# Performance work log

Measured on AMD Instinct MI355X. Metric: run time of the kernel, lower is better.

The kernel has to match this reference:

```python
import jax, jax.numpy as jnp
import numpy as np

NPOINT = 1024
RADIUS = 0.2
NSAMPLE = 32
EPS = 1e-5  # BatchNorm eps


def setup_inputs() -> dict:
    key = jax.random.key(0)
    ks = jax.random.split(key, 8)
    B, N, D = 16, 4096, 64
    xyz = jax.random.uniform(ks[0], (B, N, 3), dtype=jnp.float32)
    points = jax.random.normal(ks[1], (B, N, D), dtype=jnp.float32)
    chans = [D + 3, 64, 64, 128]  # last_channel = in_channel + 3
    inp = {"xyz": xyz, "points": points}
    for i in range(3):
        inp[f"W{i}"] = jax.random.normal(ks[2 + i], (chans[i + 1], chans[i]), dtype=jnp.float32) * 0.05
        inp[f"b{i}"] = jnp.zeros((chans[i + 1],), jnp.float32)
        inp[f"g{i}"] = jnp.ones((chans[i + 1],), jnp.float32)
        inp[f"bt{i}"] = jnp.zeros((chans[i + 1],), jnp.float32)
    return inp


def farthest_point_sample(xyz, npoint):
    # xyz: [B, N, 3] -> idx [B, npoint]. Deterministic start at index 0.
    B, N, _ = xyz.shape

    def body(carry, _):
        distance, farthest = carry
        centroid = jnp.take_along_axis(xyz, farthest[:, None, None], axis=1)  # [B,1,3]
        dist = jnp.sum((xyz - centroid) ** 2, axis=-1)  # [B,N]
        distance = jnp.minimum(distance, dist)
        nxt = jnp.argmax(distance, axis=1).astype(jnp.int32)
        return (distance, nxt), farthest

    init = (jnp.full((B, N), 1e10, xyz.dtype), jnp.zeros((B,), jnp.int32))
    _, idx = jax.lax.scan(body, init, None, length=npoint)
    return idx.T  # [B, npoint]


def query_ball_point(radius, nsample, xyz, new_xyz):
    # squared distances [B,S,N] via |a|^2 + |b|^2 - 2ab (no [B,S,N,3] blowup)
    sqr = (jnp.sum(new_xyz ** 2, -1)[:, :, None]
           + jnp.sum(xyz ** 2, -1)[:, None, :]
           - 2.0 * jnp.einsum('bsc,bnc->bsn', new_xyz, xyz))
    neg_d, idx = jax.lax.top_k(-sqr, nsample)  # k smallest dists, sorted ascending
    mask = (-neg_d) > radius ** 2
    return jnp.where(mask, idx[:, :, :1], idx)  # replace out-of-ball with nearest


def _gather(points, idx):
    # points [B,N,C], idx [B,...] -> [B,...,C]
    return jax.vmap(lambda p, i: p[i])(points, idx)


def reference(xyz, points, W0, b0, g0, bt0, W1, b1, g1, bt1, W2, b2, g2, bt2):
    fps_idx = farthest_point_sample(xyz, NPOINT)                 # [B,S]
    new_xyz = jnp.take_along_axis(xyz, fps_idx[:, :, None], axis=1)  # [B,S,3]
    idx = query_ball_point(RADIUS, NSAMPLE, xyz, new_xyz)        # [B,S,K]
    grouped_xyz = _gather(xyz, idx)                              # [B,S,K,3]
    grouped_xyz_norm = grouped_xyz - new_xyz[:, :, None, :]
    x = jnp.concatenate([grouped_xyz_norm, _gather(points, idx)], axis=-1)  # [B,S,K,C]

    # 1x1 conv + BatchNorm (training-mode batch stats over B,S,K) + ReLU
    for W, b, ga, be in ((W0, b0, g0, bt0), (W1, b1, g1, bt1), (W2, b2, g2, bt2)):
        x = jnp.einsum('bskc,oc->bsko', x, W) + b
        mu = jnp.mean(x, axis=(0, 1, 2))
        var = jnp.var(x, axis=(0, 1, 2))
        x = ga * (x - mu) * jax.lax.rsqrt(var + EPS) + be
        x = jax.nn.relu(x)

    new_points = jnp.max(x, axis=2)  # max-pool over K -> [B,S,C_out]
    return (new_xyz, new_points)
```

## Files before the change

kernel.cpp:

```cpp
#include <hip/hip_runtime.h>

typedef unsigned int u32;
typedef unsigned long long u64;
typedef unsigned short ushort_t;

#define NB 16
#define NPT 4096
#define NS 1024
#define NK 32
#define ND 64
#define CNT_TOTAL 524288.0f
#define OUT_NP_OFF 49152

__device__ __forceinline__ u64 wave_min_u64_bcast(u64 x) {
  #define DPP_MINU64(CTRL) {                                                  \
    int hi = (int)(x >> 32), lo = (int)(u32)x;                                \
    int h2 = __builtin_amdgcn_update_dpp(hi, hi, CTRL, 0xf, 0xf, false);      \
    int l2 = __builtin_amdgcn_update_dpp(lo, lo, CTRL, 0xf, 0xf, false);      \
    u64 y = ((u64)(u32)h2 << 32) | (u32)l2;                                   \
    if (y < x) x = y; }
  DPP_MINU64(0x111) DPP_MINU64(0x112) DPP_MINU64(0x114) DPP_MINU64(0x118)
  DPP_MINU64(0x142) DPP_MINU64(0x143)
  #undef DPP_MINU64
  u32 hi = (u32)__builtin_amdgcn_readlane((int)(x >> 32), 63);
  u32 lo = (u32)__builtin_amdgcn_readlane((int)(u32)x, 63);
  return ((u64)hi << 32) | lo;
}

__device__ __forceinline__ double wave_max_f64(double x) {
  #define DPP_MAXF64(CTRL) {                                                  \
    int hi = __double2hiint(x), lo = __double2loint(x);                       \
    int h2 = __builtin_amdgcn_update_dpp(hi, hi, CTRL, 0xf, 0xf, false);      \
    int l2 = __builtin_amdgcn_update_dpp(lo, lo, CTRL, 0xf, 0xf, false);      \
    x = fmax(x, __hiloint2double(h2, l2)); }
  DPP_MAXF64(0x111) DPP_MAXF64(0x112) DPP_MAXF64(0x114) DPP_MAXF64(0x118)
  DPP_MAXF64(0x142) DPP_MAXF64(0x143)
  #undef DPP_MAXF64
  return x;
}

__global__ __launch_bounds__(256) void k_fps(const float* __restrict__ xyz,
                                             float* __restrict__ out_xyz) {
  __shared__ float sx[NPT], sy[NPT], sz[NPT];
  __shared__ u64 wkey[2][4];
  const int b = blockIdx.x, t = threadIdx.x;
  const int lane = t & 63, w = t >> 6;
  const float* xb = xyz + (size_t)b * NPT * 3;
  float px[16], py[16], pz[16], dst[16];
  {
    float f[48];
    const float4* s4 = (const float4*)(xb + t * 48);
    #pragma unroll
    for (int j = 0; j < 12; ++j) {
      float4 v = s4[j];
      f[4*j+0] = v.x; f[4*j+1] = v.y; f[4*j+2] = v.z; f[4*j+3] = v.w;
    }
    #pragma unroll
    for (int k = 0; k < 16; ++k) {
      px[k] = f[3*k+0]; py[k] = f[3*k+1]; pz[k] = f[3*k+2]; dst[k] = 1e10f;
      const int n = t * 16 + k;
      sx[n] = px[k]; sy[n] = py[k]; sz[n] = pz[k];
    }
  }
  __syncthreads();
  float fx = xb[0], fy = xb[1], fz = xb[2];
  float* ob = out_xyz + (size_t)b * NS * 3;
  const int lobase = NPT - 1 - t * 16;
  for (int it = 0; it < NS; ++it) {
    if (t == 0) { ob[3*it+0] = fx; ob[3*it+1] = fy; ob[3*it+2] = fz; }
    double kk[16];
    #pragma unroll
    for (int k = 0; k < 16; ++k) {
      float dx = __fsub_rn(px[k], fx), dy = __fsub_rn(py[k], fy), dz = __fsub_rn(pz[k], fz);
      float dd = __fadd_rn(__fadd_rn(__fmul_rn(dx,dx), __fmul_rn(dy,dy)), __fmul_rn(dz,dz));
      dd = fminf(dst[k], dd);
      dst[k] = dd;
      kk[k] = __hiloint2double(__float_as_int(dd), lobase - k);
    }
    #pragma unroll
    for (int s = 8; s >= 1; s >>= 1)
      #pragma unroll
      for (int i = 0; i < 16; ++i) { if (i < s) kk[i] = fmax(kk[i], kk[i + s]); }
    double wm = wave_max_f64(kk[0]);
    const int p = it & 1;
    if (lane == 63) wkey[p][w] = ((u64)(u32)__double2hiint(wm) << 32) | (u32)__double2loint(wm);
    __syncthreads();
    u64 m0 = wkey[p][0], m1 = wkey[p][1], m2 = wkey[p][2], m3 = wkey[p][3];
    u64 ma = m0 > m1 ? m0 : m1, mb = m2 > m3 ? m2 : m3;
    u64 m = ma > mb ? ma : mb;
    const int idx = NPT - 1 - (int)(m & 0xffffffffu);
    fx = sx[idx]; fy = sy[idx]; fz = sz[idx];
  }
}

#define SQCAP 1024
__global__ __launch_bounds__(256) void k_ball(const float* __restrict__ xyz,
                                              const float* __restrict__ nxyz,
                                              ushort_t* __restrict__ ballidx) {
  __shared__ u64 keys[4][SQCAP];
  const int w = threadIdx.x >> 6, lane = threadIdx.x & 63;
  const int pair = blockIdx.x * 4 + w;
  const int b = pair >> 10;
  const float* xb = xyz + (size_t)b * NPT * 3;
  const float nx = nxyz[(size_t)pair*3+0];
  const float ny = nxyz[(size_t)pair*3+1];
  const float nz = nxyz[(size_t)pair*3+2];
  const float ssn = __fadd_rn(__fadd_rn(__fmul_rn(nx,nx), __fmul_rn(ny,ny)), __fmul_rn(nz,nz));
  int cnt = 0;
  for (int n0 = 0; n0 < NPT; n0 += 64) {
    const int n = n0 + lane;
    const float px = xb[3*n+0], py = xb[3*n+1], pz = xb[3*n+2];
    const float ssx = __fadd_rn(__fadd_rn(__fmul_rn(px,px), __fmul_rn(py,py)), __fmul_rn(pz,pz));
    const float dt  = __fadd_rn(__fadd_rn(__fmul_rn(nx,px), __fmul_rn(ny,py)), __fmul_rn(nz,pz));
    const float d   = __fsub_rn(__fadd_rn(ssn, ssx), __fmul_rn(2.0f, dt));
    const bool in = !(d > 0.04f);
    const u64 mask = __ballot(in);
    if (in) {
      int pos = cnt + (int)__popcll(mask & ((1ull << lane) - 1ull));
      if (pos < SQCAP) {
        u32 bits = __float_as_uint(d);
        u32 mapped = (bits & 0x80000000u) ? ~bits : (bits | 0x80000000u);
        keys[w][pos] = ((u64)mapped << 32) | (u32)n;
      }
    }
    cnt += (int)__popcll(mask);
  }
  if (cnt > SQCAP) cnt = SQCAP;
  ushort_t* op = ballidx + (size_t)pair * NK;
  int first = 0;
  volatile u64* kp = &keys[w][0];
  for (int iter = 0; iter < NK; ++iter) {
    if (iter < cnt) {
      u64 mb = ~0ull;
      for (int i = lane; i < cnt; i += 64) { u64 kk = kp[i]; if (kk < mb) mb = kk; }
      mb = wave_min_u64_bcast(mb);
      for (int i = lane; i < cnt; i += 64) { if (kp[i] == mb) kp[i] = ~0ull; }
      const int widx = (int)(mb & 0xffffffffu);
      if (iter == 0) first = widx;
      if (lane == 0) op[iter] = (ushort_t)widx;
    } else {
      if (lane == 0) op[iter] = (ushort_t)first;
    }
  }
}

template<int ROWS, int K, int LDW>
__device__ __forceinline__ void load_W(float* Ws, const float* __restrict__ W, int t) {
  for (int e = t; e < ROWS * K; e += 256) Ws[(e / K) * LDW + (e % K)] = W[e];
}

__device__ __forceinline__ void gather_X(float (*Xs)[69],
    const float* __restrict__ xyz, const float* __restrict__ points,
    const float* __restrict__ nxyz, const ushort_t* __restrict__ ballidx,
    int bp4, int b, int t) {
  if (t < 128) {
    const int pair = bp4 + (t >> 5);
    const int idx = (int)ballidx[pair * NK + (t & 31)];
    const float* p = xyz + ((size_t)b * NPT + idx) * 3;
    const float* nzp = nxyz + (size_t)pair * 3;
    Xs[t][0] = __fsub_rn(p[0], nzp[0]);
    Xs[t][1] = __fsub_rn(p[1], nzp[1]);
    Xs[t][2] = __fsub_rn(p[2], nzp[2]);
  }
  for (int g = t; g < 2048; g += 256) {
    const int r = g >> 4, ch = g & 15;
    const int pair = bp4 + (r >> 5);
    const int idx = (int)ballidx[pair * NK + (r & 31)];
    float4 v = *(const float4*)(points + ((size_t)b * NPT + idx) * ND + ch * 4);
    Xs[r][3 + ch*4 + 0] = v.x; Xs[r][3 + ch*4 + 1] = v.y;
    Xs[r][3 + ch*4 + 2] = v.z; Xs[r][3 + ch*4 + 3] = v.w;
  }
}

template<int K, int LDW>
__device__ __forceinline__ void gemm4(const float (*Xs)[69], const float* Ws,
                                      const float* __restrict__ bias, int biasOff,
                                      int tr, int tc, float acc[8][4]) {
  #pragma unroll
  for (int j = 0; j < 4; ++j) {
    float bb = bias[biasOff + tc*4 + j];
    #pragma unroll
    for (int i = 0; i < 8; ++i) acc[i][j] = bb;
  }
  for (int c = 0; c < K; ++c) {
    float wv[4];
    #pragma unroll
    for (int j = 0; j < 4; ++j) wv[j] = Ws[(tc*4 + j) * LDW + c];
    #pragma unroll
    for (int i = 0; i < 8; ++i) {
      float xv = Xs[tr*8 + i][c];
      #pragma unroll
      for (int j = 0; j < 4; ++j) acc[i][j] = fmaf(xv, wv[j], acc[i][j]);
    }
  }
}

__device__ __forceinline__ void bn_coef(const float* __restrict__ stats, int base,
    const float* __restrict__ g, const float* __restrict__ bt,
    float* sc, float* sh, int t) {
  if (t < 64) {
    const float inv = 1.0f / CNT_TOTAL;
    float mu = stats[base + t] * inv;
    float var = fmaxf(stats[base + 64 + t] * inv - mu * mu, 0.0f);
    float rs = rsqrtf(var + 1e-5f);
    float s = g[t] * rs;
    sc[t] = s; sh[t] = bt[t] - mu * s;
  }
}

__device__ __forceinline__ void load_y_bn(float (*Xs)[69], const float* __restrict__ y,
    size_t row0, const float* sc, const float* sh, int t) {
  for (int g = t; g < 2048; g += 256) {
    const int r = g >> 4, ch = g & 15;
    float4 v = *(const float4*)(y + (row0 + r) * 64 + ch * 4);
    const int c = ch * 4;
    Xs[r][c+0] = fmaxf(fmaf(sc[c+0], v.x, sh[c+0]), 0.0f);
    Xs[r][c+1] = fmaxf(fmaf(sc[c+1], v.y, sh[c+1]), 0.0f);
    Xs[r][c+2] = fmaxf(fmaf(sc[c+2], v.z, sh[c+2]), 0.0f);
    Xs[r][c+3] = fmaxf(fmaf(sc[c+3], v.w, sh[c+3]), 0.0f);
  }
}

__device__ __forceinline__ void bn_to_Xs(float (*Xs)[69], float acc[8][4],
    const float* sc, const float* sh, int tr, int tc) {
  #pragma unroll
  for (int j = 0; j < 4; ++j) {
    int c = tc*4 + j;
    #pragma unroll
    for (int i = 0; i < 8; ++i)
      Xs[tr*8 + i][c] = fmaxf(fmaf(sc[c], acc[i][j], sh[c]), 0.0f);
  }
}

__device__ __forceinline__ void store_y(float* __restrict__ y, size_t row0,
                                        float acc[8][4], int tr, int tc) {
  #pragma unroll
  for (int i = 0; i < 8; ++i) {
    size_t gr = row0 + tr*8 + i;
    *(float4*)(y + gr * 64 + tc*4) = make_float4(acc[i][0], acc[i][1], acc[i][2], acc[i][3]);
  }
}

__device__ __forceinline__ void stats_acc64(float acc[8][4], float* ssum, float* ssq,
    float* __restrict__ gsum, float* __restrict__ gsq, int tc, int t) {
  #pragma unroll
  for (int j = 0; j < 4; ++j) {
    float s0 = 0.f, s1 = 0.f;
    #pragma unroll
    for (int i = 0; i < 8; ++i) { s0 += acc[i][j]; s1 += acc[i][j]*acc[i][j]; }
    atomicAdd(&ssum[tc*4 + j], s0);
    atomicAdd(&ssq [tc*4 + j], s1);
  }
  __syncthreads();
  if (t < 64) { atomicAdd(&gsum[t], ssum[t]); atomicAdd(&gsq[t], ssq[t]); }
}

template<bool STORE>
__global__ __launch_bounds__(256) void k_pass0(const float* __restrict__ xyz,
    const float* __restrict__ points, const float* __restrict__ nxyz,
    const ushort_t* __restrict__ ballidx, const float* __restrict__ W0,
    const float* __restrict__ b0, float* __restrict__ y0, float* __restrict__ stats) {
  __shared__ float Xs[128][69];
  __shared__ float Ws[64*69];
  __shared__ float ssum[64], ssq[64];
  const int t = threadIdx.x;
  const int bp4 = blockIdx.x * 4, b = bp4 >> 10;
  const size_t row0 = (size_t)blockIdx.x * 128;
  if (t < 64) { ssum[t] = 0.f; ssq[t] = 0.f; }
  load_W<64,67,69>(Ws, W0, t);
  gather_X(Xs, xyz, points, nxyz, ballidx, bp4, b, t);
  __syncthreads();
  const int tr = t >> 4, tc = t & 15;
  float acc[8][4];
  gemm4<67,69>(Xs, Ws, b0, 0, tr, tc, acc);
  if (STORE) store_y(y0, row0, acc, tr, tc);
  stats_acc64(acc, ssum, ssq, stats, stats + 64, tc, t);
}

template<bool LOADY0, bool STORE>
__global__ __launch_bounds__(256) void k_pass1(const float* __restrict__ xyz,
    const float* __restrict__ points, const float* __restrict__ nxyz,
    const ushort_t* __restrict__ ballidx,
    const float* __restrict__ W0, const float* __restrict__ b0,
    const float* __restrict__ g0, const float* __restrict__ bt0,
    const float* __restrict__ W1, const float* __restrict__ b1,
    const float* __restrict__ y0, float* __restrict__ y1, float* __restrict__ stats) {
  __shared__ float Xs[128][69];
  __shared__ float Ws[64*69];
  __shared__ float sc[64], sh[64], ssum[64], ssq[64];
  const int t = threadIdx.x;
  const int bp4 = blockIdx.x * 4, b = bp4 >> 10;
  const size_t row0 = (size_t)blockIdx.x * 128;
  if (t < 64) { ssum[t] = 0.f; ssq[t] = 0.f; }
  bn_coef(stats, 0, g0, bt0, sc, sh, t);
  const int tr = t >> 4, tc = t & 15;
  if (LOADY0) {
    load_W<64,64,69>(Ws, W1, t);
    __syncthreads();
    load_y_bn(Xs, y0, row0, sc, sh, t);
    __syncthreads();
  } else {
    load_W<64,67,69>(Ws, W0, t);
    gather_X(Xs, xyz, points, nxyz, ballidx, bp4, b, t);
    __syncthreads();
    float a0[8][4];
    gemm4<67,69>(Xs, Ws, b0, 0, tr, tc, a0);
    __syncthreads();
    bn_to_Xs(Xs, a0, sc, sh, tr, tc);
    load_W<64,64,69>(Ws, W1, t);
    __syncthreads();
  }
  float acc[8][4];
  gemm4<64,69>(Xs, Ws, b1, 0, tr, tc, acc);
  if (STORE) store_y(y1, row0, acc, tr, tc);
  stats_acc64(acc, ssum, ssq, stats + 128, stats + 192, tc, t);
}

template<int MODE>
__global__ __launch_bounds__(256) void k_pass2(const float* __restrict__ xyz,
    const float* __restrict__ points, const float* __restrict__ nxyz,
    const ushort_t* __restrict__ ballidx,
    const float* __restrict__ W0, const float* __restrict__ b0,
    const float* __restrict__ g0, const float* __restrict__ bt0,
    const float* __restrict__ W1, const float* __restrict__ b1,
    const float* __restrict__ g1, const float* __restrict__ bt1,
    const float* __restrict__ W2, const float* __restrict__ b2,
    const float* __restrict__ g2,
    const float* __restrict__ y0, const float* __restrict__ y1,
    float* __restrict__ out, float* __restrict__ stats) {
  __shared__ float Xs[128][69];
  __shared__ float Ws[64*69];
  __shared__ float plex[16*64];
  __shared__ float sc0[64], sh0[64], sc1[64], sh1[64];
  __shared__ float ssum[128], ssq[128], sg[128];
  const int t = threadIdx.x;
  const int bp4 = blockIdx.x * 4, b = bp4 >> 10;
  const size_t row0 = (size_t)blockIdx.x * 128;
  if (t < 128) { ssum[t] = 0.f; ssq[t] = 0.f; sg[t] = g2[t]; }
  bn_coef(stats, 128, g1, bt1, sc1, sh1, t);
  const int tr = t >> 4, tc = t & 15;
  if (MODE == 0) {
    load_y_bn(Xs, y1, row0, sc1, sh1, t);
  } else {
    bn_coef(stats, 0, g0, bt0, sc0, sh0, t);
    if (MODE == 1) {
      load_W<64,64,69>(Ws, W1, t);
      __syncthreads();
      load_y_bn(Xs, y0, row0, sc0, sh0, t);
      __syncthreads();
    } else {
      load_W<64,67,69>(Ws, W0, t);
      gather_X(Xs, xyz, points, nxyz, ballidx, bp4, b, t);
      __syncthreads();
      float a0[8][4];
      gemm4<67,69>(Xs, Ws, b0, 0, tr, tc, a0);
      __syncthreads();
      bn_to_Xs(Xs, a0, sc0, sh0, tr, tc);
      load_W<64,64,69>(Ws, W1, t);
      __syncthreads();
    }
    float a1[8][4];
    gemm4<64,69>(Xs, Ws, b1, 0, tr, tc, a1);
    __syncthreads();
    bn_to_Xs(Xs, a1, sc1, sh1, tr, tc);
  }
  for (int h = 0; h < 2; ++h) {
    load_W<64,64,65>(Ws, W2 + h * 64 * 64, t);
    __syncthreads();
    float acc[8][4];
    gemm4<64,65>(Xs, Ws, b2, h * 64, tr, tc, acc);
    #pragma unroll
    for (int j = 0; j < 4; ++j) {
      float s0 = 0.f, s1 = 0.f;
      #pragma unroll
      for (int i = 0; i < 8; ++i) { s0 += acc[i][j]; s1 += acc[i][j]*acc[i][j]; }
      atomicAdd(&ssum[h*64 + tc*4 + j], s0);
      atomicAdd(&ssq [h*64 + tc*4 + j], s1);
    }
    #pragma unroll
    for (int j = 0; j < 4; ++j) {
      const bool useMax = sg[h*64 + tc*4 + j] >= 0.0f;
      float e = acc[0][j];
      #pragma unroll
      for (int i = 1; i < 8; ++i) e = useMax ? fmaxf(e, acc[i][j]) : fminf(e, acc[i][j]);
      plex[tr * 64 + tc*4 + j] = e;
    }
    __syncthreads();
    {
      const int pl = t >> 6, o = t & 63;
      const bool useMax = sg[h*64 + o] >= 0.0f;
      float e = plex[(pl*4 + 0) * 64 + o];
      #pragma unroll
      for (int i = 1; i < 4; ++i) {
        float v = plex[(pl*4 + i) * 64 + o];
        e = useMax ? fmaxf(e, v) : fminf(e, v);
      }
      out[OUT_NP_OFF + (size_t)(bp4 + pl) * 128 + h*64 + o] = e;
    }
  }
  __syncthreads();
  if (t < 128) { atomicAdd(&stats[256 + t], ssum[t]); atomicAdd(&stats[384 + t], ssq[t]); }
}

__global__ __launch_bounds__(256) void k_final(const float* __restrict__ stats,
                                               const float* __restrict__ g2,
                                               const float* __restrict__ bt2,
                                               float* __restrict__ out) {
  const int gid = blockIdx.x * 256 + threadIdx.x;
  const int o = gid & 127;
  const float inv = 1.0f / CNT_TOTAL;
  float mu = stats[256 + o] * inv;
  float var = fmaxf(stats[384 + o] * inv - mu * mu, 0.0f);
  float rs = rsqrtf(var + 1e-5f);
  float s = g2[o] * rs;
  float b = bt2[o] - mu * s;
  float v = out[OUT_NP_OFF + gid];
  out[OUT_NP_OFF + gid] = fmaxf(fmaf(s, v, b), 0.0f);
}

extern "C" void kernel_launch(void* const* d_in, const int* in_sizes, int n_in,
                              void* d_out, int out_size, void* d_ws, size_t ws_size,
                              hipStream_t stream) {
  (void)in_sizes; (void)n_in; (void)out_size;
  const float* xyz    = (const float*)d_in[0];
  const float* points = (const float*)d_in[1];
  const float* W0  = (const float*)d_in[2];
  const float* b0  = (const float*)d_in[3];
  const float* g0  = (const float*)d_in[4];
  const float* bt0 = (const float*)d_in[5];
  const float* W1  = (const float*)d_in[6];
  const float* b1  = (const float*)d_in[7];
  const float* g1  = (const float*)d_in[8];
  const float* bt1 = (const float*)d_in[9];
  const float* W2  = (const float*)d_in[10];
  const float* b2  = (const float*)d_in[11];
  const float* g2  = (const float*)d_in[12];
  const float* bt2 = (const float*)d_in[13];
  float* out = (float*)d_out;

  const size_t statsB = 2048;
  const size_t ballB  = (size_t)16384 * NK * 2;
  const size_t MINWS  = statsB + ballB;
  const size_t yB     = (size_t)524288 * 64 * 4;

  char* ws = (char*)d_ws;
  float* stats      = (float*)ws;
  ushort_t* ballidx = (ushort_t*)(ws + statsB);
  float* y0         = (float*)(ws + MINWS);
  float* y1         = (float*)(ws + MINWS + yB);

  hipMemsetAsync(stats, 0, statsB, stream);
  k_fps <<<dim3(NB),   dim3(256),  0, stream>>>(xyz, out);
  k_ball<<<dim3(4096), dim3(256),  0, stream>>>(xyz, out, ballidx);

  if (ws_size >= MINWS + 2 * yB) {
    k_pass0<true>        <<<dim3(4096), dim3(256), 0, stream>>>(xyz, points, out, ballidx, W0, b0, y0, stats);
    k_pass1<true, true>  <<<dim3(4096), dim3(256), 0, stream>>>(xyz, points, out, ballidx, W0, b0, g0, bt0, W1, b1, y0, y1, stats);
    k_pass2<0>           <<<dim3(4096), dim3(256), 0, stream>>>(xyz, points, out, ballidx, W0, b0, g0, bt0, W1, b1, g1, bt1, W2, b2, g2, y0, y1, out, stats);
  } else if (ws_size >= MINWS + yB) {
    k_pass0<true>        <<<dim3(4096), dim3(256), 0, stream>>>(xyz, points, out, ballidx, W0, b0, y0, stats);
    k_pass1<true, false> <<<dim3(4096), dim3(256), 0, stream>>>(xyz, points, out, ballidx, W0, b0, g0, bt0, W1, b1, y0, y1, stats);
    k_pass2<1>           <<<dim3(4096), dim3(256), 0, stream>>>(xyz, points, out, ballidx, W0, b0, g0, bt0, W1, b1, g1, bt1, W2, b2, g2, y0, y1, out, stats);
  } else {
    k_pass0<false>       <<<dim3(4096), dim3(256), 0, stream>>>(xyz, points, out, ballidx, W0, b0, y0, stats);
    k_pass1<false, false><<<dim3(4096), dim3(256), 0, stream>>>(xyz, points, out, ballidx, W0, b0, g0, bt0, W1, b1, y0, y1, stats);
    k_pass2<2>           <<<dim3(4096), dim3(256), 0, stream>>>(xyz, points, out, ballidx, W0, b0, g0, bt0, W1, b1, g1, bt1, W2, b2, g2, y0, y1, out, stats);
  }
  k_final<<<dim3(8192), dim3(256), 0, stream>>>(stats, g2, bt2, out);
}
```

Measured before the change: 1.432 ms.

## Widen FPS blocks to 512 threads and keep ball-query candidates in registers

```diff
diff --git a/kernel.cpp b/kernel.cpp
--- a/kernel.cpp
+++ b/kernel.cpp
@@ -39,38 +39,37 @@
   return x;
 }
 
-__global__ __launch_bounds__(256) void k_fps(const float* __restrict__ xyz,
+__global__ __launch_bounds__(512) void k_fps(const float* __restrict__ xyz,
                                              float* __restrict__ out_xyz) {
   __shared__ float sx[NPT], sy[NPT], sz[NPT];
-  __shared__ u64 wkey[2][4];
+  __shared__ u64 wkey[2][8];
   const int b = blockIdx.x, t = threadIdx.x;
   const int lane = t & 63, w = t >> 6;
   const float* xb = xyz + (size_t)b * NPT * 3;
-  float px[16], py[16], pz[16], dst[16];
+  float px[8], py[8], pz[8], dst[8];
   {
-    float f[48];
-    const float4* s4 = (const float4*)(xb + t * 48);
-    #pragma unroll
-    for (int j = 0; j < 12; ++j) {
-      float4 v = s4[j];
-      f[4*j+0] = v.x; f[4*j+1] = v.y; f[4*j+2] = v.z; f[4*j+3] = v.w;
-    }
-    #pragma unroll
-    for (int k = 0; k < 16; ++k) {
-      px[k] = f[3*k+0]; py[k] = f[3*k+1]; pz[k] = f[3*k+2]; dst[k] = 1e10f;
-      const int n = t * 16 + k;
+    const float4* s4 = (const float4*)(xb + t * 24);
+    float4 v0 = s4[0], v1 = s4[1], v2 = s4[2], v3 = s4[3], v4 = s4[4], v5 = s4[5];
+    px[0]=v0.x; py[0]=v0.y; pz[0]=v0.z;  px[1]=v0.w; py[1]=v1.x; pz[1]=v1.y;
+    px[2]=v1.z; py[2]=v1.w; pz[2]=v2.x;  px[3]=v2.y; py[3]=v2.z; pz[3]=v2.w;
+    px[4]=v3.x; py[4]=v3.y; pz[4]=v3.z;  px[5]=v3.w; py[5]=v4.x; pz[5]=v4.y;
+    px[6]=v4.z; py[6]=v4.w; pz[6]=v5.x;  px[7]=v5.y; py[7]=v5.z; pz[7]=v5.w;
+    #pragma unroll
+    for (int k = 0; k < 8; ++k) {
+      const int n = t * 8 + k;
       sx[n] = px[k]; sy[n] = py[k]; sz[n] = pz[k];
+      dst[k] = 1e10f;
     }
   }
   __syncthreads();
   float fx = xb[0], fy = xb[1], fz = xb[2];
   float* ob = out_xyz + (size_t)b * NS * 3;
-  const int lobase = NPT - 1 - t * 16;
+  const int lobase = NPT - 1 - t * 8;
   for (int it = 0; it < NS; ++it) {
     if (t == 0) { ob[3*it+0] = fx; ob[3*it+1] = fy; ob[3*it+2] = fz; }
-    double kk[16];
-    #pragma unroll
-    for (int k = 0; k < 16; ++k) {
+    double kk[8];
+    #pragma unroll
+    for (int k = 0; k < 8; ++k) {
       float dx = __fsub_rn(px[k], fx), dy = __fsub_rn(py[k], fy), dz = __fsub_rn(pz[k], fz);
       float dd = __fadd_rn(__fadd_rn(__fmul_rn(dx,dx), __fmul_rn(dy,dy)), __fmul_rn(dz,dz));
       dd = fminf(dst[k], dd);
@@ -78,16 +77,16 @@
       kk[k] = __hiloint2double(__float_as_int(dd), lobase - k);
     }
     #pragma unroll
-    for (int s = 8; s >= 1; s >>= 1)
+    for (int s = 4; s >= 1; s >>= 1)
       #pragma unroll
-      for (int i = 0; i < 16; ++i) { if (i < s) kk[i] = fmax(kk[i], kk[i + s]); }
+      for (int i = 0; i < 4; ++i) { if (i < s) kk[i] = fmax(kk[i], kk[i + s]); }
     double wm = wave_max_f64(kk[0]);
     const int p = it & 1;
     if (lane == 63) wkey[p][w] = ((u64)(u32)__double2hiint(wm) << 32) | (u32)__double2loint(wm);
     __syncthreads();
-    u64 m0 = wkey[p][0], m1 = wkey[p][1], m2 = wkey[p][2], m3 = wkey[p][3];
-    u64 ma = m0 > m1 ? m0 : m1, mb = m2 > m3 ? m2 : m3;
-    u64 m = ma > mb ? ma : mb;
+    u64 m = wkey[p][0];
+    #pragma unroll
+    for (int i = 1; i < 8; ++i) { u64 o = wkey[p][i]; if (o > m) m = o; }
     const int idx = NPT - 1 - (int)(m & 0xffffffffu);
     fx = sx[idx]; fy = sy[idx]; fz = sz[idx];
   }
@@ -128,18 +127,38 @@
   if (cnt > SQCAP) cnt = SQCAP;
   ushort_t* op = ballidx + (size_t)pair * NK;
   int first = 0;
-  volatile u64* kp = &keys[w][0];
-  for (int iter = 0; iter < NK; ++iter) {
-    if (iter < cnt) {
-      u64 mb = ~0ull;
-      for (int i = lane; i < cnt; i += 64) { u64 kk = kp[i]; if (kk < mb) mb = kk; }
-      mb = wave_min_u64_bcast(mb);
-      for (int i = lane; i < cnt; i += 64) { if (kp[i] == mb) kp[i] = ~0ull; }
-      const int widx = (int)(mb & 0xffffffffu);
-      if (iter == 0) first = widx;
-      if (lane == 0) op[iter] = (ushort_t)widx;
-    } else {
-      if (lane == 0) op[iter] = (ushort_t)first;
+  if (cnt <= 192) {
+    u64 r0 = (lane       < cnt) ? keys[w][lane      ] : ~0ull;
+    u64 r1 = (lane + 64  < cnt) ? keys[w][lane +  64] : ~0ull;
+    u64 r2 = (lane + 128 < cnt) ? keys[w][lane + 128] : ~0ull;
+    for (int iter = 0; iter < NK; ++iter) {
+      if (iter < cnt) {
+        u64 mb = r0 < r1 ? r0 : r1; if (r2 < mb) mb = r2;
+        mb = wave_min_u64_bcast(mb);
+        if (r0 == mb) r0 = ~0ull;
+        if (r1 == mb) r1 = ~0ull;
+        if (r2 == mb) r2 = ~0ull;
+        const int widx = (int)(mb & 0xffffffffu);
+        if (iter == 0) first = widx;
+        if (lane == 0) op[iter] = (ushort_t)widx;
+      } else {
+        if (lane == 0) op[iter] = (ushort_t)first;
+      }
+    }
+  } else {
+    volatile u64* kp = &keys[w][0];
+    for (int iter = 0; iter < NK; ++iter) {
+      if (iter < cnt) {
+        u64 mb = ~0ull;
+        for (int i = lane; i < cnt; i += 64) { u64 kk = kp[i]; if (kk < mb) mb = kk; }
+        mb = wave_min_u64_bcast(mb);
+        for (int i = lane; i < cnt; i += 64) { if (kp[i] == mb) kp[i] = ~0ull; }
+        const int widx = (int)(mb & 0xffffffffu);
+        if (iter == 0) first = widx;
+        if (lane == 0) op[iter] = (ushort_t)widx;
+      } else {
+        if (lane == 0) op[iter] = (ushort_t)first;
+      }
     }
   }
 }
@@ -450,7 +469,7 @@
   float* y1         = (float*)(ws + MINWS + yB);
 
   hipMemsetAsync(stats, 0, statsB, stream);
-  k_fps <<<dim3(NB),   dim3(256),  0, stream>>>(xyz, out);
+  k_fps <<<dim3(NB),   dim3(512),  0, stream>>>(xyz, out);
   k_ball<<<dim3(4096), dim3(256),  0, stream>>>(xyz, out, ballidx);
 
   if (ws_size >= MINWS + 2 * yB) {
```

Result: no change. 1.423 ms (-0.6%).
